# Kernel tuning notes

Measured on AMD Instinct MI355X. Metric: run time of the kernel, lower is better.

Reference implementation:

```python
import jax, jax.numpy as jnp
import numpy as np

D_MODEL = 1024
QK_DIM = 1024
V_DIM = 1024
H = 16
TAU = 20.0
HQK = QK_DIM // H
HV = V_DIM // H
SCALE = HQK ** -0.5
SCALE_BASE = 512.0
EPS_GAMMA = 1e-8
EPS_GN = 1e-5


def _rotate_every_two(x):
    x1 = x[..., ::2]
    x2 = x[..., 1::2]
    return jnp.stack([-x2, x1], axis=-1).reshape(x.shape)


def _xpos_rotate(q, k, t):
    # q,k: (B,H,N,d); t: (B,N) continuous positions (timestamps in days)
    d = q.shape[-1]
    inv_freq = (1.0 / (10000.0 ** (np.arange(0, d, 2) / d))).astype(np.float32)  # (d/2,)
    sinusoid = t[:, None, :, None] * inv_freq  # (B,1,N,d/2)
    sin = jnp.repeat(jnp.sin(sinusoid), 2, axis=-1)  # (B,1,N,d)
    cos = jnp.repeat(jnp.cos(sinusoid), 2, axis=-1)
    scale_vec = ((np.arange(0, d, 2) + 0.4 * d) / (1.4 * d)).astype(np.float32)  # (d/2,)
    scale = jnp.repeat(scale_vec ** (t[:, None, :, None] / SCALE_BASE), 2, axis=-1)  # (B,1,N,d)
    q_rot = (q * cos + _rotate_every_two(q) * sin) * scale
    k_rot = (k * cos + _rotate_every_two(k) * sin) / scale
    return q_rot, k_rot


def setup_inputs() -> dict:
    key = jax.random.key(0)
    ks = jax.random.split(key, 6)
    B, N = 4, 1024
    X = jax.random.normal(ks[0], (B, N, D_MODEL), dtype=jnp.float32)
    # increasing timestamps in days
    timestamps = jnp.sort(jax.random.uniform(ks[1], (B, N), jnp.float32, 0.0, 100.0), axis=-1)
    W_qkv = jax.random.normal(ks[2], (D_MODEL, 2 * QK_DIM + V_DIM), dtype=jnp.float32) * 0.02
    W_gamma = jax.random.normal(ks[3], (D_MODEL, H), dtype=jnp.float32) * 0.02
    W_gated = jax.random.normal(ks[4], (D_MODEL, V_DIM), dtype=jnp.float32) * 0.02
    W_out = jax.random.normal(ks[5], (V_DIM, D_MODEL), dtype=jnp.float32) * 0.02
    return {"X": X, "timestamps": timestamps, "W_qkv": W_qkv, "W_gamma": W_gamma,
            "W_gated": W_gated, "W_out": W_out}


def reference(X, timestamps, W_qkv, W_gamma, W_gated, W_out):
    B, N, _ = X.shape
    qkv = X @ W_qkv  # (B,N,2*qk+v)
    q, k, v = jnp.split(qkv, [QK_DIM, 2 * QK_DIM], axis=-1)
    q = q.reshape(B, N, H, HQK).transpose(0, 2, 1, 3)  # (B,H,N,dk)
    k = k.reshape(B, N, H, HQK).transpose(0, 2, 1, 3)
    v = v.reshape(B, N, H, HV).transpose(0, 2, 1, 3)
    q, k = _xpos_rotate(q, k, timestamps)
    # data-dependent decay gamma in (0,1]
    gamma = jax.nn.sigmoid(X @ W_gamma) ** (1.0 / TAU)  # (B,N,H)
    log_b = jnp.cumsum(jnp.log(gamma + EPS_GAMMA), axis=1).transpose(0, 2, 1)  # (B,H,N)
    log_D = log_b[..., :, None] - log_b[..., None, :]  # (B,H,N,N)
    causal = jnp.tril(jnp.ones((N, N), dtype=bool))
    # masked_fill(-inf) then clamp[-80,0]: clip maps -inf -> -80 (matches torch)
    D = jnp.exp(jnp.clip(jnp.where(causal, log_D, -jnp.inf), -80.0, 0.0))
    attn = jnp.einsum('bhnd,bhmd->bhnm', q, k) * SCALE * D
    O = jnp.einsum('bhnm,bhmd->bhnd', attn, v)  # (B,H,N,dv)
    O = O.transpose(0, 2, 1, 3).reshape(B, N, V_DIM)
    # GroupNorm(num_groups=H, affine=False) over (channels-in-group, seq)
    g = O.reshape(B, N, H, HV)
    mu = g.mean(axis=(1, 3), keepdims=True)
    var = g.var(axis=(1, 3), keepdims=True)
    O = ((g - mu) / jnp.sqrt(var + EPS_GN)).reshape(B, N, V_DIM)
    O = jax.nn.silu(X @ W_gated) * O
    return O @ W_out
```

## Files before the change

### kernel.cpp

```cpp
#include <hip/hip_runtime.h>
#include <cstddef>
#include <cstdint>

#define NH 16
#define HD 64
#define NSEQ 1024
#define NB 4
#define DM 1024
#define SCALE 0.125f

typedef __attribute__((ext_vector_type(8))) short v8s;
typedef __attribute__((ext_vector_type(4))) float v4f;

__device__ __forceinline__ short f2bf(float x) {
    union { float f; unsigned u; } v; v.f = x;
    unsigned r = v.u + 0x7FFF + ((v.u >> 16) & 1);
    return (short)(r >> 16);
}
__device__ __forceinline__ float bf2f(short x) {
    union { unsigned u; float f; } v; v.u = ((unsigned)(unsigned short)x) << 16;
    return v.f;
}
__device__ __forceinline__ void gload16(const void* g, void* l) {
    __builtin_amdgcn_global_load_lds(
        (const __attribute__((address_space(1))) void*)g,
        (__attribute__((address_space(3))) void*)l, 16, 0, 0);
}
__device__ __forceinline__ int gswz(int r, int kbyte) {
    return (r * 64 + kbyte) ^ (((r >> 1) & 3) << 4);
}
__device__ __forceinline__ int aswz(int r, int byte) {
    return (r * 128 + byte) ^ ((r & 7) << 4);
}
#define SBAR() __builtin_amdgcn_s_barrier()
#define WAITV0() asm volatile("s_waitcnt vmcnt(0)" ::: "memory")
#define WAITV4() asm volatile("s_waitcnt vmcnt(4)" ::: "memory")
#define WAITL() asm volatile("s_waitcnt lgkmcnt(0)" ::: "memory")

__global__ __launch_bounds__(256) void convert_rows(const float* __restrict__ X,
                                                    short* __restrict__ Xb, int K) {
    const int kt = blockIdx.x, rt = blockIdx.y;
    const int t = threadIdx.x;
    const int rloc = t >> 1, kb0 = (t & 1) * 16;
    const float* src = X + (size_t)(rt * 128 + rloc) * K + kt * 32 + kb0;
    short o[16] __attribute__((aligned(16)));
#pragma unroll
    for (int j = 0; j < 16; j += 4) {
        float4 v = *(const float4*)(src + j);
        o[j] = f2bf(v.x); o[j + 1] = f2bf(v.y); o[j + 2] = f2bf(v.z); o[j + 3] = f2bf(v.w);
    }
    char* base = (char*)(Xb + ((size_t)rt * (K >> 5) + kt) * 4096);
#pragma unroll
    for (int c = 0; c < 2; ++c)
        *(v8s*)(base + gswz(rloc, kb0 * 2 + c * 16)) = *(v8s*)&o[c * 8];
}

__global__ __launch_bounds__(256) void tconv(const float* __restrict__ W,
                                             short* __restrict__ Bt,
                                             int K, int N) {
    __shared__ short lsm[32][136];
    const int ct = blockIdx.x, kt = blockIdx.y;
    const int t = threadIdx.x;
    {
        const int kk = t >> 3, nn0 = (t & 7) * 16;
        const float* src = W + (size_t)(kt * 32 + kk) * N + ct * 128 + nn0;
#pragma unroll
        for (int j = 0; j < 16; j += 4) {
            float4 v = *(const float4*)(src + j);
            lsm[kk][nn0 + j] = f2bf(v.x); lsm[kk][nn0 + j + 1] = f2bf(v.y);
            lsm[kk][nn0 + j + 2] = f2bf(v.z); lsm[kk][nn0 + j + 3] = f2bf(v.w);
        }
    }
    __syncthreads();
    const int rloc = t >> 1, kb0 = (t & 1) * 16;
    short o[16] __attribute__((aligned(16)));
#pragma unroll
    for (int j = 0; j < 16; ++j) o[j] = lsm[kb0 + j][rloc];
    char* base = (char*)(Bt + ((size_t)ct * (K >> 5) + kt) * 4096);
#pragma unroll
    for (int c = 0; c < 2; ++c)
        *(v8s*)(base + gswz(rloc, kb0 * 2 + c * 16)) = *(v8s*)&o[c * 8];
}

template<int MODE>
__global__ __launch_bounds__(256) void gemm_tt(const short* __restrict__ A,
                                               const short* __restrict__ B,
                                               void* __restrict__ C, int N,
                                               const float* __restrict__ O,
                                               const float* __restrict__ stats) {
    __shared__ short As[4096];
    __shared__ short Bs[4096];
    const int tid = threadIdx.x;
    const int w = tid >> 6, l = tid & 63;
    const int wr = w >> 1, wc = w & 1;
    const int rt = blockIdx.y, ct = blockIdx.x;
    const char* Abase = (const char*)A + ((size_t)rt * 32) * 8192;
    const char* Bbase = (const char*)B + ((size_t)ct * 32) * 8192;

    v4f acc[4][4];
#pragma unroll
    for (int i = 0; i < 4; ++i)
#pragma unroll
        for (int j = 0; j < 4; ++j) acc[i][j] = (v4f){0.f, 0.f, 0.f, 0.f};

    for (int kt = 0; kt < 32; ++kt) {
        __syncthreads();
#pragma unroll
        for (int i = 0; i < 2; ++i) {
            const int c = w * 2 + i;
            gload16(Abase + (size_t)kt * 8192 + c * 1024 + l * 16, (char*)As + c * 1024);
            gload16(Bbase + (size_t)kt * 8192 + c * 1024 + l * 16, (char*)Bs + c * 1024);
        }
        __syncthreads();
        v8s af[4], bfr[4];
#pragma unroll
        for (int i = 0; i < 4; ++i) {
            const int ra = wr * 64 + i * 16 + (l & 15);
            af[i] = *(const v8s*)((char*)As + gswz(ra, (l >> 4) * 16));
            const int rb = wc * 64 + i * 16 + (l & 15);
            bfr[i] = *(const v8s*)((char*)Bs + gswz(rb, (l >> 4) * 16));
        }
#pragma unroll
        for (int i = 0; i < 4; ++i)
#pragma unroll
            for (int j = 0; j < 4; ++j)
                acc[i][j] = __builtin_amdgcn_mfma_f32_16x16x32_bf16(af[i], bfr[j], acc[i][j], 0, 0, 0);
    }
    float mu = 0.f, rstd = 0.f;
    if (MODE == 2) {
        const int hh = ct * 2 + wc;
        mu   = stats[((rt >> 3) * NH + hh) * 2];
        rstd = stats[((rt >> 3) * NH + hh) * 2 + 1];
    }
#pragma unroll
    for (int i = 0; i < 4; ++i)
#pragma unroll
        for (int j = 0; j < 4; ++j) {
            const int r0 = rt * 128 + wr * 64 + i * 16 + (l >> 4) * 4;
            const int cc = ct * 128 + wc * 64 + j * 16 + (l & 15);
#pragma unroll
            for (int t2 = 0; t2 < 4; ++t2) {
                if (MODE == 1) ((short*)C)[(size_t)(r0 + t2) * N + cc] = f2bf(acc[i][j][t2]);
                else if (MODE == 0) ((float*)C)[(size_t)(r0 + t2) * N + cc] = acc[i][j][t2];
                else {
                    const int row = r0 + t2;
                    const float g = acc[i][j][t2];
                    const float silu = g / (1.0f + __expf(-g));
                    const float ov = O[(size_t)row * DM + cc];
                    const float val = silu * (ov - mu) * rstd;
                    const int rloc = row - rt * 128;
                    char* base = (char*)((short*)C + ((size_t)rt * 32 + (cc >> 5)) * 4096);
                    *(short*)(base + gswz(rloc, (cc & 31) * 2)) = f2bf(val);
                }
            }
        }
}

__global__ __launch_bounds__(256) void gamma2(const float* __restrict__ X,
                                              const float* __restrict__ Wg,
                                              float* __restrict__ loggam) {
    __shared__ float wgs[1024 * 17];
    const int tid = threadIdx.x;
#pragma unroll
    for (int it = 0; it < 16; ++it) {
        const int idx = it * 1024 + tid * 4;
        float4 v = *(const float4*)(Wg + idx);
        const int k = idx >> 4, h0 = idx & 15;
        wgs[k * 17 + h0]     = v.x;
        wgs[k * 17 + h0 + 1] = v.y;
        wgs[k * 17 + h0 + 2] = v.z;
        wgs[k * 17 + h0 + 3] = v.w;
    }
    __syncthreads();

    const int r = tid >> 4, c = tid & 15;
    const int row = blockIdx.x * 16 + r;
    const float* xrow = X + (size_t)row * DM;
    float acc[16];
#pragma unroll
    for (int h = 0; h < 16; ++h) acc[h] = 0.0f;
#pragma unroll 4
    for (int i = 0; i < 16; ++i) {
        const int kb = i * 64 + c * 4;
        float4 xv = *(const float4*)(xrow + kb);
        const float xs[4] = {xv.x, xv.y, xv.z, xv.w};
#pragma unroll
        for (int j = 0; j < 4; ++j) {
            const float* wrow = &wgs[(kb + j) * 17];
#pragma unroll
            for (int h = 0; h < 16; ++h) acc[h] = fmaf(xs[j], wrow[h], acc[h]);
        }
    }
#pragma unroll
    for (int h = 0; h < 16; ++h) {
#pragma unroll
        for (int off = 8; off >= 1; off >>= 1)
            acc[h] += __shfl_xor(acc[h], off, 16);
    }
    const float d = acc[c];
    const float sig = 1.0f / (1.0f + expf(-d));
    const float gam = powf(sig, 1.0f / 20.0f);
    loggam[(size_t)row * NH + c] = logf(gam + 1e-8f);
}

__global__ __launch_bounds__(256) void scan_kernel(const float* __restrict__ lg,
                                                   float* __restrict__ lgT) {
    const int wave = threadIdx.x >> 6;
    const int lane = threadIdx.x & 63;
    const int bh = blockIdx.x * 4 + wave;
    const int b = bh >> 4, h = bh & 15;
    const float* p = lg + (size_t)b * NSEQ * NH + h;
    const int n0 = lane * 16;
    float v[16];
    float s = 0.0f;
#pragma unroll
    for (int j = 0; j < 16; ++j) { v[j] = p[(size_t)(n0 + j) * NH]; s += v[j]; }
    float sc = s;
#pragma unroll
    for (int off = 1; off < 64; off <<= 1) {
        float o = __shfl_up(sc, off, 64);
        if (lane >= off) sc += o;
    }
    float acc = sc - s;
    float* q = lgT + (size_t)bh * NSEQ + n0;
#pragma unroll
    for (int j = 0; j < 16; ++j) { acc += v[j]; q[j] = acc; }
}

__global__ __launch_bounds__(256) void prep(const short* __restrict__ qkvb,
                                            const float* __restrict__ ts,
                                            short* __restrict__ Qb,
                                            short* __restrict__ Kb,
                                            short* __restrict__ Vtb) {
    __shared__ short vsm[64][72];
    const int tile = blockIdx.x, bh = blockIdx.y;
    const int b = bh >> 4, h = bh & 15;
    const int t = threadIdx.x;
    const int rloc = t >> 2, d0 = (t & 3) * 16;
    const int row = b * NSEQ + tile * 64 + rloc;
    const short* src = qkvb + (size_t)row * 3072 + h * HD;
    const size_t tb = ((size_t)bh * 16 + tile) * 4096;

    float qa[16], ka[16];
    {
        v8s q0 = *(const v8s*)(src + d0), q1 = *(const v8s*)(src + d0 + 8);
        v8s k0 = *(const v8s*)(src + 1024 + d0), k1 = *(const v8s*)(src + 1024 + d0 + 8);
#pragma unroll
        for (int j = 0; j < 8; ++j) {
            qa[j] = bf2f(q0[j]); qa[j + 8] = bf2f(q1[j]);
            ka[j] = bf2f(k0[j]); ka[j + 8] = bf2f(k1[j]);
        }
    }
    const float tv = ts[row];
    short qo[16] __attribute__((aligned(16)));
    short ko[16] __attribute__((aligned(16)));
#pragma unroll
    for (int j = 0; j < 8; ++j) {
        const int i = (d0 >> 1) + j;
        const float inv_freq = exp2f(-0.4152410119f * (float)i);
        const float ang = tv * inv_freq;
        const float s = sinf(ang), c = cosf(ang);
        const float sv = ((float)(2 * i) + 25.6f) * (1.0f / 89.6f);
        const float e = log2f(sv) * tv * (1.0f / 512.0f);
        const float sc = exp2f(e) * SCALE, isc = exp2f(-e);
        qo[2 * j]     = f2bf((qa[2 * j] * c - qa[2 * j + 1] * s) * sc);
        qo[2 * j + 1] = f2bf((qa[2 * j + 1] * c + qa[2 * j] * s) * sc);
        ko[2 * j]     = f2bf((ka[2 * j] * c - ka[2 * j + 1] * s) * isc);
        ko[2 * j + 1] = f2bf((ka[2 * j + 1] * c + ka[2 * j] * s) * isc);
    }
#pragma unroll
    for (int c = 0; c < 2; ++c) {
        *(v8s*)((char*)(Qb + tb) + aswz(rloc, d0 * 2 + c * 16)) = *(v8s*)&qo[c * 8];
        *(v8s*)((char*)(Kb + tb) + aswz(rloc, d0 * 2 + c * 16)) = *(v8s*)&ko[c * 8];
    }
    {
        v8s v0 = *(const v8s*)(src + 2048 + d0), v1 = *(const v8s*)(src + 2048 + d0 + 8);
        *(short4*)&vsm[rloc][d0]      = *(short4*)&v0;
        *(short4*)&vsm[rloc][d0 + 4]  = *((short4*)&v0 + 1);
        *(short4*)&vsm[rloc][d0 + 8]  = *(short4*)&v1;
        *(short4*)&vsm[rloc][d0 + 12] = *((short4*)&v1 + 1);
    }
    __syncthreads();
    {
        const int d = t >> 2, m0 = (t & 3) * 16;
        short vt[16] __attribute__((aligned(16)));
#pragma unroll
        for (int j = 0; j < 16; ++j) vt[j] = vsm[m0 + j][d];
#pragma unroll
        for (int c = 0; c < 2; ++c)
            *(v8s*)((char*)(Vtb + tb) + aswz(d, m0 * 2 + c * 16)) = *(v8s*)&vt[c * 8];
    }
}

__global__ __launch_bounds__(256) void attn5(const short* __restrict__ Qb,
                                             const short* __restrict__ Kb,
                                             const short* __restrict__ Vtb,
                                             const float* __restrict__ logbT,
                                             float* __restrict__ O,
                                             float* __restrict__ partial) {
    __shared__ short Ks[2][4096];
    __shared__ short Vts[2][4096];
    __shared__ short Ps[8192];
    __shared__ float lbAll[1024];
    __shared__ float emAll[1024];
    const int id = blockIdx.x;
    const int half = id >> 8;
    const int idx = id & 255;
    const int bh = ((idx & 7) << 3) | ((idx >> 3) & 7);
    const int qq = half == 0 ? (4 + (idx >> 6)) : (3 - (idx >> 6));
    const int b = bh >> 4, h = bh & 15;
    const int tid = threadIdx.x;
    const int w = tid >> 6, l = tid & 63;
    const int n0 = qq * 128;
    const int NT = 2 * qq + 2;

#pragma unroll
    for (int i = 0; i < 4; ++i) {
        const int c = w * 4 + i;
        gload16((const char*)Qb + ((size_t)bh * 16 + 2 * qq) * 8192 + c * 1024 + l * 16,
                (char*)Ps + c * 1024);
    }
    for (int i = tid; i < 1024; i += 256)
        lbAll[i] = logbT[(size_t)bh * NSEQ + i];
    WAITV0(); WAITL();
    SBAR();

    const float base = lbAll[n0];
    for (int i = tid; i < NT * 64; i += 256) emAll[i] = __expf(base - lbAll[i]);
    float en[2];
#pragma unroll
    for (int rg = 0; rg < 2; ++rg)
        en[rg] = __expf(lbAll[n0 + w * 32 + rg * 16 + (l & 15)] - base);
    v8s aq[2][2];
#pragma unroll
    for (int rg = 0; rg < 2; ++rg)
#pragma unroll
        for (int kc = 0; kc < 2; ++kc) {
            const int r = w * 32 + rg * 16 + (l & 15);
            aq[rg][kc] = *(const v8s*)((char*)Ps + (r >> 6) * 8192 +
                                       aswz(r & 63, kc * 64 + (l >> 4) * 16));
        }
    WAITL();
    SBAR();

    v4f oacc[2][4];
#pragma unroll
    for (int rg = 0; rg < 2; ++rg)
#pragma unroll
        for (int dt = 0; dt < 4; ++dt) oacc[rg][dt] = (v4f){0.f, 0.f, 0.f, 0.f};

#pragma unroll
    for (int i = 0; i < 2; ++i) {
        const int c = w * 2 + i;
        gload16((const char*)Kb + ((size_t)bh * 16 + 0) * 8192 + c * 1024 + l * 16,
                (char*)Ks + c * 1024);
        gload16((const char*)Vtb + ((size_t)bh * 16 + 0) * 8192 + c * 1024 + l * 16,
                (char*)Vts + c * 1024);
    }

    for (int t = 0; t < NT; ++t) {
        const int m0 = t * 64;
        const int buf = t & 1;
        SBAR();
        if (t + 1 < NT) {
            const int nb = (t + 1) & 1;
#pragma unroll
            for (int i = 0; i < 2; ++i) {
                const int c = w * 2 + i;
                gload16((const char*)Kb + ((size_t)bh * 16 + t + 1) * 8192 + c * 1024 + l * 16,
                        (char*)Ks + nb * 8192 + c * 1024);
                gload16((const char*)Vtb + ((size_t)bh * 16 + t + 1) * 8192 + c * 1024 + l * 16,
                        (char*)Vts + nb * 8192 + c * 1024);
            }
            WAITV4();
        } else {
            WAITV0();
        }
        SBAR();

        const bool active = (m0 <= n0 + w * 32 + 31);
        if (active) {
            const char* KsB = (const char*)Ks + buf * 8192;
            const char* VtsB = (const char*)Vts + buf * 8192;
            v4f sfr[2][4];
#pragma unroll
            for (int rg = 0; rg < 2; ++rg)
#pragma unroll
                for (int m4 = 0; m4 < 4; ++m4) sfr[rg][m4] = (v4f){0.f, 0.f, 0.f, 0.f};
#pragma unroll
            for (int m4 = 0; m4 < 4; ++m4) {
#pragma unroll
                for (int kc = 0; kc < 2; ++kc) {
                    const int m = m4 * 16 + (l & 15);
                    v8s bk = *(const v8s*)(KsB + aswz(m, kc * 64 + (l >> 4) * 16));
#pragma unroll
                    for (int rg = 0; rg < 2; ++rg)
                        sfr[rg][m4] = __builtin_amdgcn_mfma_f32_16x16x32_bf16(bk, aq[rg][kc], sfr[rg][m4], 0, 0, 0);
                }
            }
            const bool needMask = (m0 + 63) > (n0 + w * 32);
#pragma unroll
            for (int rg = 0; rg < 2; ++rg) {
                const int r = w * 32 + rg * 16 + (l & 15);
                const float enr = en[rg];
#pragma unroll
                for (int m4 = 0; m4 < 4; ++m4) {
                    const int mbase = m0 + m4 * 16 + (l >> 4) * 4;
                    float4 emv = *(const float4*)&emAll[mbase];
                    const float ems[4] = {emv.x, emv.y, emv.z, emv.w};
                    union { short s[4]; uint2 u; } pk;
#pragma unroll
                    for (int t2 = 0; t2 < 4; ++t2) {
                        float sval = sfr[rg][m4][t2] * enr * ems[t2];
                        if (needMask && (n0 + r) < (mbase + t2)) sval = 0.0f;
                        pk.s[t2] = f2bf(sval);
                    }
                    *(uint2*)((char*)Ps + aswz(r, (m4 * 16 + (l >> 4) * 4) * 2)) = pk.u;
                }
            }
            WAITL();
            __builtin_amdgcn_sched_barrier(0);
#pragma unroll
            for (int kc = 0; kc < 2; ++kc) {
                v8s ap[2];
#pragma unroll
                for (int rg = 0; rg < 2; ++rg) {
                    const int r = w * 32 + rg * 16 + (l & 15);
                    ap[rg] = *(const v8s*)((char*)Ps + aswz(r, kc * 64 + (l >> 4) * 16));
                }
#pragma unroll
                for (int dt = 0; dt < 4; ++dt) {
                    const int d = dt * 16 + (l & 15);
                    v8s bv = *(const v8s*)(VtsB + aswz(d, kc * 64 + (l >> 4) * 16));
#pragma unroll
                    for (int rg = 0; rg < 2; ++rg)
                        oacc[rg][dt] = __builtin_amdgcn_mfma_f32_16x16x32_bf16(bv, ap[rg], oacc[rg][dt], 0, 0, 0);
                }
            }
        }
    }
    float psum = 0.0f, pssq = 0.0f;
#pragma unroll
    for (int rg = 0; rg < 2; ++rg) {
        const int row = n0 + w * 32 + rg * 16 + (l & 15);
#pragma unroll
        for (int dt = 0; dt < 4; ++dt) {
            const float4 v = {oacc[rg][dt][0], oacc[rg][dt][1], oacc[rg][dt][2], oacc[rg][dt][3]};
            *(float4*)(O + (size_t)(b * NSEQ + row) * DM + h * HD + dt * 16 + (l >> 4) * 4) = v;
            psum += v.x + v.y + v.z + v.w;
            pssq += v.x * v.x + v.y * v.y + v.z * v.z + v.w * v.w;
        }
    }
    __syncthreads();
    float* red = (float*)Ks;
    red[tid] = psum; red[256 + tid] = pssq;
    __syncthreads();
    for (int s = 128; s > 0; s >>= 1) {
        if (tid < s) { red[tid] += red[tid + s]; red[256 + tid] += red[256 + tid + s]; }
        __syncthreads();
    }
    if (tid == 0) {
        partial[(bh * 8 + qq) * 2]     = red[0];
        partial[(bh * 8 + qq) * 2 + 1] = red[256];
    }
}

__global__ __launch_bounds__(64) void gn_finalize(const float* __restrict__ partial,
                                                  float* __restrict__ stats) {
    const int bh = threadIdx.x;
    float s = 0.0f, q = 0.0f;
#pragma unroll
    for (int i = 0; i < 8; ++i) {
        s += partial[(bh * 8 + i) * 2];
        q += partial[(bh * 8 + i) * 2 + 1];
    }
    const float inv = 1.0f / (NSEQ * HD);
    const float mu = s * inv;
    const float var = q * inv - mu * mu;
    stats[bh * 2] = mu;
    stats[bh * 2 + 1] = rsqrtf(var + 1e-5f);
}

extern "C" void kernel_launch(void* const* d_in, const int* in_sizes, int n_in,
                              void* d_out, int out_size, void* d_ws, size_t ws_size,
                              hipStream_t stream) {
    const float* X       = (const float*)d_in[0];
    const float* ts      = (const float*)d_in[1];
    const float* W_qkv   = (const float*)d_in[2];
    const float* W_gamma = (const float*)d_in[3];
    const float* W_gated = (const float*)d_in[4];
    const float* W_out   = (const float*)d_in[5];
    float* out = (float*)d_out;

    char* ws = (char*)d_ws;
    short* qkvb = (short*)ws;
    float* logb = (float*)(ws + 25165824);
    float* Oatt = (float*)(ws + 25427968);
    float* stats = (float*)(ws + 42205184);
    short* Xb   = (short*)(ws + 42205696);
    short* Wtq  = (short*)(ws + 50594304);
    short* Wtg  = (short*)(ws + 56885760);
    short* Wto  = (short*)(ws + 58982912);
    short* Qb   = (short*)(ws + 61080064);
    short* Kb   = (short*)(ws + 69468672);
    short* Vtb  = (short*)(ws + 77857280);
    float* logbT = (float*)(ws + 86245888);
    short* Gb   = Xb;
    float* partial = (float*)Wtq;

    convert_rows<<<dim3(32, 32), 256, 0, stream>>>(X, Xb, 1024);
    tconv<<<dim3(24, 32), 256, 0, stream>>>(W_qkv, Wtq, 1024, 3072);
    tconv<<<dim3(8, 32), 256, 0, stream>>>(W_gated, Wtg, 1024, 1024);
    tconv<<<dim3(8, 32), 256, 0, stream>>>(W_out, Wto, 1024, 1024);

    gemm_tt<1><<<dim3(24, 32), 256, 0, stream>>>(Xb, Wtq, qkvb, 3072, nullptr, nullptr);
    gamma2<<<256, 256, 0, stream>>>(X, W_gamma, logb);
    scan_kernel<<<16, 256, 0, stream>>>(logb, logbT);
    prep<<<dim3(16, 64), 256, 0, stream>>>(qkvb, ts, Qb, Kb, Vtb);
    attn5<<<512, 256, 0, stream>>>(Qb, Kb, Vtb, logbT, Oatt, partial);
    gn_finalize<<<1, 64, 0, stream>>>(partial, stats);
    gemm_tt<2><<<dim3(8, 32), 256, 0, stream>>>(Xb, Wtg, Gb, 1024, Oatt, stats);
    gemm_tt<0><<<dim3(8, 32), 256, 0, stream>>>(Gb, Wto, out, 1024, nullptr, nullptr);
}
```

Before: 164.6 us.

## Merge conversion kernels, fold GN finalize into gemm, store attention output as bf16

The three weight transpose-convert launches become one kernel, and the X bf16 conversion moves into the gamma projection kernel. The GroupNorm finalize kernel is removed; each gated-GEMM block now reduces the partial sums itself. The attention output is written as bf16 instead of fp32, halving that write and the later read. setprio hints are added around the MFMA loops in attention. Together these cut launch count and memory traffic, at the cost of slight extra rounding error on O and some redundant stat reductions.

```diff
diff --git a/kernel.cpp b/kernel.cpp
--- a/kernel.cpp
+++ b/kernel.cpp
@@ -37,29 +37,19 @@
 #define WAITV4() asm volatile("s_waitcnt vmcnt(4)" ::: "memory")
 #define WAITL() asm volatile("s_waitcnt lgkmcnt(0)" ::: "memory")
 
-__global__ __launch_bounds__(256) void convert_rows(const float* __restrict__ X,
-                                                    short* __restrict__ Xb, int K) {
-    const int kt = blockIdx.x, rt = blockIdx.y;
-    const int t = threadIdx.x;
-    const int rloc = t >> 1, kb0 = (t & 1) * 16;
-    const float* src = X + (size_t)(rt * 128 + rloc) * K + kt * 32 + kb0;
-    short o[16] __attribute__((aligned(16)));
-#pragma unroll
-    for (int j = 0; j < 16; j += 4) {
-        float4 v = *(const float4*)(src + j);
-        o[j] = f2bf(v.x); o[j + 1] = f2bf(v.y); o[j + 2] = f2bf(v.z); o[j + 3] = f2bf(v.w);
-    }
-    char* base = (char*)(Xb + ((size_t)rt * (K >> 5) + kt) * 4096);
-#pragma unroll
-    for (int c = 0; c < 2; ++c)
-        *(v8s*)(base + gswz(rloc, kb0 * 2 + c * 16)) = *(v8s*)&o[c * 8];
-}
-
-__global__ __launch_bounds__(256) void tconv(const float* __restrict__ W,
-                                             short* __restrict__ Bt,
-                                             int K, int N) {
+__global__ __launch_bounds__(256) void tconv3(const float* __restrict__ Wq,
+                                              const float* __restrict__ Wgt,
+                                              const float* __restrict__ Wo,
+                                              short* __restrict__ Wtq,
+                                              short* __restrict__ Wtg,
+                                              short* __restrict__ Wto) {
     __shared__ short lsm[32][136];
-    const int ct = blockIdx.x, kt = blockIdx.y;
+    int ct = blockIdx.x;
+    const int kt = blockIdx.y;
+    const float* W; short* Bt; int N;
+    if (ct < 24)      { W = Wq;  Bt = Wtq; N = 3072; }
+    else if (ct < 32) { W = Wgt; Bt = Wtg; N = 1024; ct -= 24; }
+    else              { W = Wo;  Bt = Wto; N = 1024; ct -= 32; }
     const int t = threadIdx.x;
     {
         const int kk = t >> 3, nn0 = (t & 7) * 16;
@@ -76,7 +66,7 @@
     short o[16] __attribute__((aligned(16)));
 #pragma unroll
     for (int j = 0; j < 16; ++j) o[j] = lsm[kb0 + j][rloc];
-    char* base = (char*)(Bt + ((size_t)ct * (K >> 5) + kt) * 4096);
+    char* base = (char*)(Bt + ((size_t)ct * 32 + kt) * 4096);
 #pragma unroll
     for (int c = 0; c < 2; ++c)
         *(v8s*)(base + gswz(rloc, kb0 * 2 + c * 16)) = *(v8s*)&o[c * 8];
@@ -86,8 +76,8 @@
 __global__ __launch_bounds__(256) void gemm_tt(const short* __restrict__ A,
                                                const short* __restrict__ B,
                                                void* __restrict__ C, int N,
-                                               const float* __restrict__ O,
-                                               const float* __restrict__ stats) {
+                                               const short* __restrict__ O,
+                                               const float* __restrict__ partial) {
     __shared__ short As[4096];
     __shared__ short Bs[4096];
     const int tid = threadIdx.x;
@@ -129,8 +119,16 @@
     float mu = 0.f, rstd = 0.f;
     if (MODE == 2) {
         const int hh = ct * 2 + wc;
-        mu   = stats[((rt >> 3) * NH + hh) * 2];
-        rstd = stats[((rt >> 3) * NH + hh) * 2 + 1];
+        const int bh = (rt >> 3) * NH + hh;
+        float s = 0.f, q = 0.f;
+#pragma unroll
+        for (int i = 0; i < 8; ++i) {
+            s += partial[(bh * 8 + i) * 2];
+            q += partial[(bh * 8 + i) * 2 + 1];
+        }
+        const float inv = 1.0f / (NSEQ * HD);
+        mu = s * inv;
+        rstd = rsqrtf(q * inv - mu * mu + 1e-5f);
     }
 #pragma unroll
     for (int i = 0; i < 4; ++i)
@@ -146,7 +144,7 @@
                     const int row = r0 + t2;
                     const float g = acc[i][j][t2];
                     const float silu = g / (1.0f + __expf(-g));
-                    const float ov = O[(size_t)row * DM + cc];
+                    const float ov = bf2f(O[(size_t)row * DM + cc]);
                     const float val = silu * (ov - mu) * rstd;
                     const int rloc = row - rt * 128;
                     char* base = (char*)((short*)C + ((size_t)rt * 32 + (cc >> 5)) * 4096);
@@ -156,9 +154,10 @@
         }
 }
 
-__global__ __launch_bounds__(256) void gamma2(const float* __restrict__ X,
-                                              const float* __restrict__ Wg,
-                                              float* __restrict__ loggam) {
+__global__ __launch_bounds__(256) void gamma_conv(const float* __restrict__ X,
+                                                  const float* __restrict__ Wg,
+                                                  float* __restrict__ loggam,
+                                                  short* __restrict__ Xb) {
     __shared__ float wgs[1024 * 17];
     const int tid = threadIdx.x;
 #pragma unroll
@@ -175,6 +174,8 @@
 
     const int r = tid >> 4, c = tid & 15;
     const int row = blockIdx.x * 16 + r;
+    const int rt = row >> 7, rloc = row & 127;
+    char* xtile = (char*)(Xb + (size_t)rt * 32 * 4096);
     const float* xrow = X + (size_t)row * DM;
     float acc[16];
 #pragma unroll
@@ -183,6 +184,8 @@
     for (int i = 0; i < 16; ++i) {
         const int kb = i * 64 + c * 4;
         float4 xv = *(const float4*)(xrow + kb);
+        short4 o4 = make_short4(f2bf(xv.x), f2bf(xv.y), f2bf(xv.z), f2bf(xv.w));
+        *(short4*)(xtile + (size_t)(kb >> 5) * 8192 + gswz(rloc, (kb & 31) * 2)) = o4;
         const float xs[4] = {xv.x, xv.y, xv.z, xv.w};
 #pragma unroll
         for (int j = 0; j < 4; ++j) {
@@ -292,11 +295,11 @@
     }
 }
 
-__global__ __launch_bounds__(256) void attn5(const short* __restrict__ Qb,
+__global__ __launch_bounds__(256) void attn6(const short* __restrict__ Qb,
                                              const short* __restrict__ Kb,
                                              const short* __restrict__ Vtb,
                                              const float* __restrict__ logbT,
-                                             float* __restrict__ O,
+                                             short* __restrict__ O,
                                              float* __restrict__ partial) {
     __shared__ short Ks[2][4096];
     __shared__ short Vts[2][4096];
@@ -387,6 +390,7 @@
             for (int rg = 0; rg < 2; ++rg)
 #pragma unroll
                 for (int m4 = 0; m4 < 4; ++m4) sfr[rg][m4] = (v4f){0.f, 0.f, 0.f, 0.f};
+            __builtin_amdgcn_s_setprio(1);
 #pragma unroll
             for (int m4 = 0; m4 < 4; ++m4) {
 #pragma unroll
@@ -398,6 +402,7 @@
                         sfr[rg][m4] = __builtin_amdgcn_mfma_f32_16x16x32_bf16(bk, aq[rg][kc], sfr[rg][m4], 0, 0, 0);
                 }
             }
+            __builtin_amdgcn_s_setprio(0);
             const bool needMask = (m0 + 63) > (n0 + w * 32);
 #pragma unroll
             for (int rg = 0; rg < 2; ++rg) {
@@ -420,6 +425,7 @@
             }
             WAITL();
             __builtin_amdgcn_sched_barrier(0);
+            __builtin_amdgcn_s_setprio(1);
 #pragma unroll
             for (int kc = 0; kc < 2; ++kc) {
                 v8s ap[2];
@@ -437,6 +443,7 @@
                         oacc[rg][dt] = __builtin_amdgcn_mfma_f32_16x16x32_bf16(bv, ap[rg], oacc[rg][dt], 0, 0, 0);
                 }
             }
+            __builtin_amdgcn_s_setprio(0);
         }
     }
     float psum = 0.0f, pssq = 0.0f;
@@ -445,10 +452,12 @@
         const int row = n0 + w * 32 + rg * 16 + (l & 15);
 #pragma unroll
         for (int dt = 0; dt < 4; ++dt) {
-            const float4 v = {oacc[rg][dt][0], oacc[rg][dt][1], oacc[rg][dt][2], oacc[rg][dt][3]};
-            *(float4*)(O + (size_t)(b * NSEQ + row) * DM + h * HD + dt * 16 + (l >> 4) * 4) = v;
-            psum += v.x + v.y + v.z + v.w;
-            pssq += v.x * v.x + v.y * v.y + v.z * v.z + v.w * v.w;
+            const float a0 = oacc[rg][dt][0], a1 = oacc[rg][dt][1];
+            const float a2 = oacc[rg][dt][2], a3 = oacc[rg][dt][3];
+            short4 o4 = make_short4(f2bf(a0), f2bf(a1), f2bf(a2), f2bf(a3));
+            *(short4*)(O + (size_t)(b * NSEQ + row) * DM + h * HD + dt * 16 + (l >> 4) * 4) = o4;
+            psum += a0 + a1 + a2 + a3;
+            pssq += a0 * a0 + a1 * a1 + a2 * a2 + a3 * a3;
         }
     }
     __syncthreads();
@@ -463,22 +472,6 @@
         partial[(bh * 8 + qq) * 2]     = red[0];
         partial[(bh * 8 + qq) * 2 + 1] = red[256];
     }
-}
-
-__global__ __launch_bounds__(64) void gn_finalize(const float* __restrict__ partial,
-                                                  float* __restrict__ stats) {
-    const int bh = threadIdx.x;
-    float s = 0.0f, q = 0.0f;
-#pragma unroll
-    for (int i = 0; i < 8; ++i) {
-        s += partial[(bh * 8 + i) * 2];
-        q += partial[(bh * 8 + i) * 2 + 1];
-    }
-    const float inv = 1.0f / (NSEQ * HD);
-    const float mu = s * inv;
-    const float var = q * inv - mu * mu;
-    stats[bh * 2] = mu;
-    stats[bh * 2 + 1] = rsqrtf(var + 1e-5f);
 }
 
 extern "C" void kernel_launch(void* const* d_in, const int* in_sizes, int n_in,
@@ -495,8 +488,7 @@
     char* ws = (char*)d_ws;
     short* qkvb = (short*)ws;
     float* logb = (float*)(ws + 25165824);
-    float* Oatt = (float*)(ws + 25427968);
-    float* stats = (float*)(ws + 42205184);
+    short* Oatt = (short*)(ws + 25427968);
     short* Xb   = (short*)(ws + 42205696);
     short* Wtq  = (short*)(ws + 50594304);
     short* Wtg  = (short*)(ws + 56885760);
@@ -508,17 +500,12 @@
     short* Gb   = Xb;
     float* partial = (float*)Wtq;
 
-    convert_rows<<<dim3(32, 32), 256, 0, stream>>>(X, Xb, 1024);
-    tconv<<<dim3(24, 32), 256, 0, stream>>>(W_qkv, Wtq, 1024, 3072);
-    tconv<<<dim3(8, 32), 256, 0, stream>>>(W_gated, Wtg, 1024, 1024);
-    tconv<<<dim3(8, 32), 256, 0, stream>>>(W_out, Wto, 1024, 1024);
-
+    tconv3<<<dim3(40, 32), 256, 0, stream>>>(W_qkv, W_gated, W_out, Wtq, Wtg, Wto);
+    gamma_conv<<<256, 256, 0, stream>>>(X, W_gamma, logb, Xb);
     gemm_tt<1><<<dim3(24, 32), 256, 0, stream>>>(Xb, Wtq, qkvb, 3072, nullptr, nullptr);
-    gamma2<<<256, 256, 0, stream>>>(X, W_gamma, logb);
     scan_kernel<<<16, 256, 0, stream>>>(logb, logbT);
     prep<<<dim3(16, 64), 256, 0, stream>>>(qkvb, ts, Qb, Kb, Vtb);
-    attn5<<<512, 256, 0, stream>>>(Qb, Kb, Vtb, logbT, Oatt, partial);
-    gn_finalize<<<1, 64, 0, stream>>>(partial, stats);
-    gemm_tt<2><<<dim3(8, 32), 256, 0, stream>>>(Xb, Wtg, Gb, 1024, Oatt, stats);
+    attn6<<<512, 256, 0, stream>>>(Qb, Kb, Vtb, logbT, Oatt, partial);
+    gemm_tt<2><<<dim3(8, 32), 256, 0, stream>>>(Xb, Wtg, Gb, 1024, Oatt, partial);
     gemm_tt<0><<<dim3(8, 32), 256, 0, stream>>>(Gb, Wto, out, 1024, nullptr, nullptr);
 }
```

New measurement: 154.1 us. 1.07x faster.
